# Kernel optimization log

Hardware: AMD Instinct MI355X
Metric: run time of the kernel (lower is better)

## Reference

```python
import jax, jax.numpy as jnp
import numpy as np

S, B, H, K = 2048, 64, 8, 12          # seq_len, input_bits, num_heads, bits per RAM neuron
N_POS = 11                             # bits for relative distance in [0, max_seq_len-1]


def setup_inputs() -> dict:
    key = jax.random.key(0)
    k1, k2, k3, k4, k5 = jax.random.split(key, 5)
    tokens = jax.random.randint(k1, (S, B), 0, 2, dtype=jnp.int32)            # bit tokens
    conn_heads = jax.random.randint(k2, (H, K), 0, 2 * B + N_POS, dtype=jnp.int32)
    head_table = jnp.round(jax.random.uniform(k3, (H, 1 << K))).astype(jnp.float32)  # {0,1} RAM cells
    conn_v = jax.random.randint(k4, (B, K), 0, B, dtype=jnp.int32)
    table_v = jnp.round(jax.random.uniform(k5, (B, 1 << K))).astype(jnp.float32)     # {0,1} RAM cells
    return {"tokens": tokens, "conn_heads": conn_heads, "head_table": head_table,
            "conn_v": conn_v, "table_v": table_v}


def reference(tokens, conn_heads, head_table, conn_v, table_v):
    pow2 = (1 << (K - 1 - jnp.arange(K))).astype(jnp.int32)                 # [K] MSB-first
    tok = tokens.astype(jnp.int32)                                           # [S,B]

    # split each head's 12 connections into query / key / relative-position groups
    grp_q = (conn_heads < B).astype(jnp.int32)
    grp_k = ((conn_heads >= B) & (conn_heads < 2 * B)).astype(jnp.int32)
    grp_p = (conn_heads >= 2 * B).astype(jnp.int32)
    cq = jnp.clip(conn_heads, 0, B - 1)
    ck = jnp.clip(conn_heads - B, 0, B - 1)
    cp = jnp.clip(conn_heads - 2 * B, 0, N_POS - 1)

    # additive address decomposition: addr(i,j,h) = addr_q(i,h)+addr_k(j,h)+addr_p(i-j,h)
    addr_q = (tok[:, cq] * (grp_q * pow2)[None]).sum(-1)                     # [S,H]
    addr_k = (tok[:, ck] * (grp_k * pow2)[None]).sum(-1)                     # [S,H]
    ar = jnp.arange(S)
    posb = ((ar[:, None] >> (N_POS - 1 - jnp.arange(N_POS))[None, :]) & 1).astype(jnp.int32)  # [S,N_POS]
    addr_p = (posb[:, cp] * (grp_p * pow2)[None]).sum(-1)                    # [S,H] indexed by rel dist

    rel = jnp.clip(ar[:, None] - ar[None, :], 0)                             # [S,S]
    addr = addr_q[:, None, :] + addr_k[None, :, :] + addr_p[rel]             # [S,S,H]

    # per-head table lookup, sum over heads = vote counts
    votes = head_table[jnp.arange(H)[None, None, :], addr].sum(-1)           # [S,S]
    causal = ar[None, :] <= ar[:, None]
    votes = jnp.where(causal, votes, 0.0)

    # bit-level value projection: one RAM neuron per output bit
    addr_v = (tok[:, conn_v] * pow2[None, None, :]).sum(-1)                  # [S,B]
    values = table_v[jnp.arange(B)[None, :], addr_v]                         # [S,B]

    # TOP_1 aggregation: first key with max vote; zeros if max vote is 0
    max_vote = votes.max(axis=1)                                             # [S]
    best = jnp.argmax(votes, axis=1)                                         # first occurrence, like the loop
    out = jnp.where((max_vote > 0)[:, None], values[best], 0.0)              # [S,B]
    return out
```

## Files before the change

kernel.cpp:

```cpp
#include <hip/hip_runtime.h>


#define SS 2048
#define BB 64
#define HH 8
#define KK 12
#define NPOS 11
#define TBL 4096
#define TBLW (TBL / 32)

typedef unsigned short u16;
typedef unsigned int u32;


__global__ __launch_bounds__(256) void precompute_kernel(
    const int* __restrict__ tokens,
    const int* __restrict__ conn_heads,
    const float* __restrict__ head_table,
    u16* __restrict__ A16, u16* __restrict__ AK16, u16* __restrict__ P16,
    u32* __restrict__ bits)
{
    int gid = blockIdx.x * blockDim.x + threadIdx.x;
    if (gid < SS * HH) {
        int s = gid >> 3;
        int h = gid & 7;
        int aq = 0, ak = 0, ap = 0;
        #pragma unroll
        for (int k = 0; k < KK; ++k) {
            int c = conn_heads[h * KK + k];
            int sh = KK - 1 - k;
            if (c < BB) {
                aq |= (tokens[s * BB + c] & 1) << sh;
            } else if (c < 2 * BB) {
                ak |= (tokens[s * BB + (c - BB)] & 1) << sh;
            } else {
                int cp = c - 2 * BB;
                ap |= ((s >> (NPOS - 1 - cp)) & 1) << sh;
            }
        }
        A16[gid]  = (u16)aq;
        AK16[gid] = (u16)ak;
        P16[gid]  = (u16)ap;
    } else {
        int w = gid - SS * HH;
        if (w < HH * TBLW) {
            int h = w >> 7;
            int wi = w & (TBLW - 1);
            u32 bv = 0;
            #pragma unroll
            for (int b = 0; b < 32; ++b) {
                if (head_table[h * TBL + wi * 32 + b] > 0.5f) bv |= (1u << b);
            }
            bits[w] = bv;
        }
    }
}

__device__ __forceinline__ int votes_packed(const u32* sbits,
                                            const uint4& q, const uint4& kk, const uint4& pp)
{
    int v = 0;
    u32 w, a0, a1;
    w = q.x | kk.x | pp.x;
    a0 = w & 0xFFFFu; a1 = w >> 16;
    v += (sbits[0 * TBLW + (a0 >> 5)] >> (a0 & 31)) & 1;
    v += (sbits[1 * TBLW + (a1 >> 5)] >> (a1 & 31)) & 1;
    w = q.y | kk.y | pp.y;
    a0 = w & 0xFFFFu; a1 = w >> 16;
    v += (sbits[2 * TBLW + (a0 >> 5)] >> (a0 & 31)) & 1;
    v += (sbits[3 * TBLW + (a1 >> 5)] >> (a1 & 31)) & 1;
    w = q.z | kk.z | pp.z;
    a0 = w & 0xFFFFu; a1 = w >> 16;
    v += (sbits[4 * TBLW + (a0 >> 5)] >> (a0 & 31)) & 1;
    v += (sbits[5 * TBLW + (a1 >> 5)] >> (a1 & 31)) & 1;
    w = q.w | kk.w | pp.w;
    a0 = w & 0xFFFFu; a1 = w >> 16;
    v += (sbits[6 * TBLW + (a0 >> 5)] >> (a0 & 31)) & 1;
    v += (sbits[7 * TBLW + (a1 >> 5)] >> (a1 & 31)) & 1;
    return v;
}

__global__ __launch_bounds__(256) void vote_kernel(
    const u16* __restrict__ A16, const u16* __restrict__ AK16, const u16* __restrict__ P16,
    const u32* __restrict__ bits_g,
    const int* __restrict__ tokens,
    const int* __restrict__ conn_v,
    const float* __restrict__ table_v,
    float* __restrict__ out)
{
    __shared__ u32 sbits[HH * TBLW];
    __shared__ u32 skey[2][4];
    __shared__ int sdone[2];

    const int tid = threadIdx.x;
    const int b = blockIdx.x;
    const int i0 = b;
    const int i1 = SS - 1 - b;

    ((uint4*)sbits)[tid] = ((const uint4*)bits_g)[tid];
    if (tid == 0) { sdone[0] = 0; sdone[1] = 0; }
    __syncthreads();

    const uint4 q0 = *(const uint4*)(A16 + i0 * HH);
    const uint4 q1 = *(const uint4*)(A16 + i1 * HH);

    u32 key0 = 0u, key1 = 0u;
    int done0 = 0, done1 = 0;
    const int nc0 = (i0 >> 8) + 1;
    const int nc1 = (i1 >> 8) + 1;

    for (int c = 0; ; ++c) {
        const int j = (c << 8) + tid;
        int f0 = 0, f1 = 0;
        if (!done0 && j <= i0) {
            const uint4 kk = *(const uint4*)(AK16 + j * HH);
            const uint4 pp = *(const uint4*)(P16 + (i0 - j) * HH);
            int v = votes_packed(sbits, q0, kk, pp);
            u32 key = ((u32)v << 12) | (u32)(4095 - j);
            key0 = key0 > key ? key0 : key;
            f0 = (v == HH);
        }
        if (!done1 && j <= i1) {
            const uint4 kk = *(const uint4*)(AK16 + j * HH);
            const uint4 pp = *(const uint4*)(P16 + (i1 - j) * HH);
            int v = votes_packed(sbits, q1, kk, pp);
            u32 key = ((u32)v << 12) | (u32)(4095 - j);
            key1 = key1 > key ? key1 : key;
            f1 = (v == HH);
        }
        if (f0) sdone[0] = 1;
        if (f1) sdone[1] = 1;
        __syncthreads();
        const int d0 = sdone[0], d1 = sdone[1];
        __syncthreads();
        done0 = d0 | ((c + 1) >= nc0);
        done1 = d1 | ((c + 1) >= nc1);
        if (done0 && done1) break;
    }

    #pragma unroll
    for (int off = 32; off > 0; off >>= 1) {
        u32 o0 = (u32)__shfl_xor((int)key0, off, 64);
        u32 o1 = (u32)__shfl_xor((int)key1, off, 64);
        key0 = key0 > o0 ? key0 : o0;
        key1 = key1 > o1 ? key1 : o1;
    }
    if ((tid & 63) == 0) {
        skey[0][tid >> 6] = key0;
        skey[1][tid >> 6] = key1;
    }
    __syncthreads();

    if (tid < 128) {
        const int r = tid >> 6;
        const int lane = tid & 63;
        u32 ka = skey[r][0] > skey[r][1] ? skey[r][0] : skey[r][1];
        u32 kb = skey[r][2] > skey[r][3] ? skey[r][2] : skey[r][3];
        u32 kf = ka > kb ? ka : kb;
        const int row = r ? i1 : i0;
        float o = 0.0f;
        if ((kf >> 12) > 0) {
            const int best = 4095 - (int)(kf & 4095u);
            int av = 0;
            #pragma unroll
            for (int k = 0; k < KK; ++k) {
                int c = conn_v[lane * KK + k];
                av |= (tokens[best * BB + c] & 1) << (KK - 1 - k);
            }
            o = table_v[lane * TBL + av];
        }
        out[row * BB + lane] = o;
    }
}

extern "C" void kernel_launch(void* const* d_in, const int* in_sizes, int n_in,
                              void* d_out, int out_size, void* d_ws, size_t ws_size,
                              hipStream_t stream) {
    const int*   tokens     = (const int*)d_in[0];
    const int*   conn_heads = (const int*)d_in[1];
    const float* head_table = (const float*)d_in[2];
    const int*   conn_v     = (const int*)d_in[3];
    const float* table_v    = (const float*)d_in[4];
    float* out = (float*)d_out;

    int* ws = (int*)d_ws;
    u16* A16  = (u16*)ws;
    u16* AK16 = (u16*)(ws + 1 * SS * HH / 2);
    u16* P16  = (u16*)(ws + 2 * SS * HH / 2);
    u32* bits = (u32*)(ws + 3 * SS * HH / 2);

    const int total1 = SS * HH + HH * TBLW;
    precompute_kernel<<<(total1 + 255) / 256, 256, 0, stream>>>(
        tokens, conn_heads, head_table, A16, AK16, P16, bits);
    vote_kernel<<<SS / 2, 256, 0, stream>>>(
        A16, AK16, P16, bits, tokens, conn_v, table_v, out);
}
```

Measured before the change: 72.69 us.

## Fuse precompute and vote kernels into one cooperative launch with grid sync

Merges the address/bit-table precompute kernel into the vote kernel using a cooperative launch and a grid-wide sync, removing one kernel launch and the gap between the two kernels. It also double-buffers the early-exit flags by loop parity so one __syncthreads per chunk can be dropped. The grid sync adds its own cost, and the cooperative launch requires all 1024 blocks to be co-resident, which the launch bounds of 4 blocks per CU are meant to allow.

```diff
diff --git a/kernel.cpp b/kernel.cpp
--- a/kernel.cpp
+++ b/kernel.cpp
@@ -1,4 +1,7 @@
 #include <hip/hip_runtime.h>
+#include <hip/hip_cooperative_groups.h>
+
+namespace cg = cooperative_groups;
 
 
 #define SS 2048
@@ -11,50 +14,6 @@
 
 typedef unsigned short u16;
 typedef unsigned int u32;
-
-
-__global__ __launch_bounds__(256) void precompute_kernel(
-    const int* __restrict__ tokens,
-    const int* __restrict__ conn_heads,
-    const float* __restrict__ head_table,
-    u16* __restrict__ A16, u16* __restrict__ AK16, u16* __restrict__ P16,
-    u32* __restrict__ bits)
-{
-    int gid = blockIdx.x * blockDim.x + threadIdx.x;
-    if (gid < SS * HH) {
-        int s = gid >> 3;
-        int h = gid & 7;
-        int aq = 0, ak = 0, ap = 0;
-        #pragma unroll
-        for (int k = 0; k < KK; ++k) {
-            int c = conn_heads[h * KK + k];
-            int sh = KK - 1 - k;
-            if (c < BB) {
-                aq |= (tokens[s * BB + c] & 1) << sh;
-            } else if (c < 2 * BB) {
-                ak |= (tokens[s * BB + (c - BB)] & 1) << sh;
-            } else {
-                int cp = c - 2 * BB;
-                ap |= ((s >> (NPOS - 1 - cp)) & 1) << sh;
-            }
-        }
-        A16[gid]  = (u16)aq;
-        AK16[gid] = (u16)ak;
-        P16[gid]  = (u16)ap;
-    } else {
-        int w = gid - SS * HH;
-        if (w < HH * TBLW) {
-            int h = w >> 7;
-            int wi = w & (TBLW - 1);
-            u32 bv = 0;
-            #pragma unroll
-            for (int b = 0; b < 32; ++b) {
-                if (head_table[h * TBL + wi * 32 + b] > 0.5f) bv |= (1u << b);
-            }
-            bits[w] = bv;
-        }
-    }
-}
 
 __device__ __forceinline__ int votes_packed(const u32* sbits,
                                             const uint4& q, const uint4& kk, const uint4& pp)
@@ -80,25 +39,65 @@
     return v;
 }
 
-__global__ __launch_bounds__(256) void vote_kernel(
-    const u16* __restrict__ A16, const u16* __restrict__ AK16, const u16* __restrict__ P16,
-    const u32* __restrict__ bits_g,
+__global__ __launch_bounds__(256, 4) void fused_kernel(
     const int* __restrict__ tokens,
+    const int* __restrict__ conn_heads,
+    const float* __restrict__ head_table,
     const int* __restrict__ conn_v,
     const float* __restrict__ table_v,
+    u16* __restrict__ A16, u16* __restrict__ AK16, u16* __restrict__ P16,
+    u32* __restrict__ bits_g,
     float* __restrict__ out)
 {
+    const int tid = threadIdx.x;
+    const int b = blockIdx.x;
+
+    {
+        int gid = b * 256 + tid;
+        if (gid < SS * HH) {
+            int s = gid >> 3;
+            int h = gid & 7;
+            int aq = 0, ak = 0, ap = 0;
+            #pragma unroll
+            for (int k = 0; k < KK; ++k) {
+                int c = conn_heads[h * KK + k];
+                int sh = KK - 1 - k;
+                if (c < BB) {
+                    aq |= (tokens[s * BB + c] & 1) << sh;
+                } else if (c < 2 * BB) {
+                    ak |= (tokens[s * BB + (c - BB)] & 1) << sh;
+                } else {
+                    int cp = c - 2 * BB;
+                    ap |= ((s >> (NPOS - 1 - cp)) & 1) << sh;
+                }
+            }
+            A16[gid]  = (u16)aq;
+            AK16[gid] = (u16)ak;
+            P16[gid]  = (u16)ap;
+        } else if (gid < SS * HH + HH * TBLW) {
+            int w = gid - SS * HH;
+            int h = w >> 7;
+            int wi = w & (TBLW - 1);
+            u32 bv = 0;
+            #pragma unroll
+            for (int bb = 0; bb < 32; ++bb) {
+                if (head_table[h * TBL + wi * 32 + bb] > 0.5f) bv |= (1u << bb);
+            }
+            bits_g[w] = bv;
+        }
+    }
+
+    cg::this_grid().sync();
+
     __shared__ u32 sbits[HH * TBLW];
     __shared__ u32 skey[2][4];
-    __shared__ int sdone[2];
+    __shared__ int sdone[2][2];
 
-    const int tid = threadIdx.x;
-    const int b = blockIdx.x;
     const int i0 = b;
     const int i1 = SS - 1 - b;
 
     ((uint4*)sbits)[tid] = ((const uint4*)bits_g)[tid];
-    if (tid == 0) { sdone[0] = 0; sdone[1] = 0; }
+    if (tid < 4) ((int*)sdone)[tid] = 0;
     __syncthreads();
 
     const uint4 q0 = *(const uint4*)(A16 + i0 * HH);
@@ -111,6 +110,7 @@
 
     for (int c = 0; ; ++c) {
         const int j = (c << 8) + tid;
+        const int par = c & 1;
         int f0 = 0, f1 = 0;
         if (!done0 && j <= i0) {
             const uint4 kk = *(const uint4*)(AK16 + j * HH);
@@ -128,13 +128,11 @@
             key1 = key1 > key ? key1 : key;
             f1 = (v == HH);
         }
-        if (f0) sdone[0] = 1;
-        if (f1) sdone[1] = 1;
+        if (f0) sdone[0][par] = 1;
+        if (f1) sdone[1][par] = 1;
         __syncthreads();
-        const int d0 = sdone[0], d1 = sdone[1];
-        __syncthreads();
-        done0 = d0 | ((c + 1) >= nc0);
-        done1 = d1 | ((c + 1) >= nc1);
+        done0 |= sdone[0][par] | ((c + 1) >= nc0);
+        done1 |= sdone[1][par] | ((c + 1) >= nc1);
         if (done0 && done1) break;
     }
 
@@ -189,9 +187,12 @@
     u16* P16  = (u16*)(ws + 2 * SS * HH / 2);
     u32* bits = (u32*)(ws + 3 * SS * HH / 2);
 
-    const int total1 = SS * HH + HH * TBLW;
-    precompute_kernel<<<(total1 + 255) / 256, 256, 0, stream>>>(
-        tokens, conn_heads, head_table, A16, AK16, P16, bits);
-    vote_kernel<<<SS / 2, 256, 0, stream>>>(
-        A16, AK16, P16, bits, tokens, conn_v, table_v, out);
+    void* args[] = {
+        (void*)&tokens, (void*)&conn_heads, (void*)&head_table,
+        (void*)&conn_v, (void*)&table_v,
+        (void*)&A16, (void*)&AK16, (void*)&P16, (void*)&bits,
+        (void*)&out
+    };
+    hipLaunchCooperativeKernel((void*)fused_kernel, dim3(SS / 2), dim3(256),
+                               args, 0, stream);
 }
```

New measurement: 148.0 us. 104% more time.

## Replace early-exit vote loop with fixed balanced row-pair sweep

Applied to the files above, without the earlier changes.

Removes the shared-memory early-termination flag and its two barriers per chunk. Each block now covers the combined 2049 causal keys of its row pair (i0, SS-1-i0) in exactly 8 fully unrolled iterations plus one extra element, with no divergence between rows. This drops barrier and branch overhead and balances work across blocks. In exchange it gives up the early exit when a row reaches the maximum vote, so every causal key is always evaluated.

```diff
diff --git a/kernel.cpp b/kernel.cpp
--- a/kernel.cpp
+++ b/kernel.cpp
@@ -11,7 +11,6 @@
 
 typedef unsigned short u16;
 typedef unsigned int u32;
-
 
 __global__ __launch_bounds__(256) void precompute_kernel(
     const int* __restrict__ tokens,
@@ -90,7 +89,6 @@
 {
     __shared__ u32 sbits[HH * TBLW];
     __shared__ u32 skey[2][4];
-    __shared__ int sdone[2];
 
     const int tid = threadIdx.x;
     const int b = blockIdx.x;
@@ -98,44 +96,33 @@
     const int i1 = SS - 1 - b;
 
     ((uint4*)sbits)[tid] = ((const uint4*)bits_g)[tid];
-    if (tid == 0) { sdone[0] = 0; sdone[1] = 0; }
     __syncthreads();
 
     const uint4 q0 = *(const uint4*)(A16 + i0 * HH);
     const uint4 q1 = *(const uint4*)(A16 + i1 * HH);
 
     u32 key0 = 0u, key1 = 0u;
-    int done0 = 0, done1 = 0;
-    const int nc0 = (i0 >> 8) + 1;
-    const int nc1 = (i1 >> 8) + 1;
 
-    for (int c = 0; ; ++c) {
-        const int j = (c << 8) + tid;
-        int f0 = 0, f1 = 0;
-        if (!done0 && j <= i0) {
-            const uint4 kk = *(const uint4*)(AK16 + j * HH);
-            const uint4 pp = *(const uint4*)(P16 + (i0 - j) * HH);
-            int v = votes_packed(sbits, q0, kk, pp);
-            u32 key = ((u32)v << 12) | (u32)(4095 - j);
-            key0 = key0 > key ? key0 : key;
-            f0 = (v == HH);
-        }
-        if (!done1 && j <= i1) {
-            const uint4 kk = *(const uint4*)(AK16 + j * HH);
-            const uint4 pp = *(const uint4*)(P16 + (i1 - j) * HH);
-            int v = votes_packed(sbits, q1, kk, pp);
-            u32 key = ((u32)v << 12) | (u32)(4095 - j);
-            key1 = key1 > key ? key1 : key;
-            f1 = (v == HH);
-        }
-        if (f0) sdone[0] = 1;
-        if (f1) sdone[1] = 1;
-        __syncthreads();
-        const int d0 = sdone[0], d1 = sdone[1];
-        __syncthreads();
-        done0 = d0 | ((c + 1) >= nc0);
-        done1 = d1 | ((c + 1) >= nc1);
-        if (done0 && done1) break;
+    #pragma unroll
+    for (int it = 0; it < 8; ++it) {
+        const int c = (it << 8) + tid;
+        const bool r0 = (c <= i0);
+        const int j = r0 ? c : (c - i0 - 1);
+        const int d = r0 ? (i0 - c) : (2048 - c);
+        const uint4 kk = *(const uint4*)(AK16 + j * HH);
+        const uint4 pp = *(const uint4*)(P16 + d * HH);
+        const uint4 q = r0 ? q0 : q1;
+        const int v = votes_packed(sbits, q, kk, pp);
+        const u32 key = ((u32)v << 12) | (u32)(4095 - j);
+        if (r0) { key0 = key0 > key ? key0 : key; }
+        else    { key1 = key1 > key ? key1 : key; }
+    }
+    if (tid == 0) {
+        const uint4 kk = *(const uint4*)(AK16 + i1 * HH);
+        const uint4 pp = *(const uint4*)(P16);
+        const int v = votes_packed(sbits, q1, kk, pp);
+        const u32 key = ((u32)v << 12) | (u32)(4095 - i1);
+        key1 = key1 > key ? key1 : key;
     }
 
     #pragma unroll
```

Result: no change. 72.32 us (-0.5%).
